# Performance work log

Measured on AMD Instinct MI355X. Metric: run time of the kernel, lower is better.

## Reference

```python
import jax, jax.numpy as jnp
import numpy as np

H = 4096
IN = 512
OUT = 64


def setup_inputs() -> dict:
    key = jax.random.key(0)
    ks = jax.random.split(key, 10)
    return {
        "inp": jax.random.normal(ks[0], (1, IN), jnp.float32),
        "hidden": jax.random.normal(ks[1], (1, H), jnp.float32),
        "hebb": jax.random.normal(ks[2], (H, H), jnp.float32) * 0.01,
        "W_i2h": jax.random.normal(ks[3], (H, IN), jnp.float32) * (1.0 / np.sqrt(IN)),
        "b_i2h": jax.random.normal(ks[4], (H,), jnp.float32),
        "w": jax.random.uniform(ks[5], (H, H), jnp.float32) * 0.01,
        "plas": jax.random.uniform(ks[6], (H, H), jnp.float32) * 0.01,
        "learn": jnp.full((1,), 0.01, jnp.float32),
        "W_h2o": jax.random.normal(ks[7], (OUT, H), jnp.float32) * (1.0 / np.sqrt(H)),
        "b_h2o": jax.random.normal(ks[8], (OUT,), jnp.float32),
    }


def reference(inp, hidden, hebb, W_i2h, b_i2h, w, plas, learn, W_h2o, b_h2o):
    # plastic-Miconi, rule='hebb', activ='relu'
    # x = relu(i2h(input) + hidden @ (w + plas * hebb))   [1, H]
    pre = inp @ W_i2h.T + b_i2h + hidden @ (w + plas * hebb)
    x = jax.nn.relu(pre)
    # hebb <- (1 - learn) * hebb + learn * outer(hidden, x)   [H, H]
    hebb_new = (1.0 - learn) * hebb + learn * (hidden.T @ x)
    # output = tanh(h2o(x))   [1, OUT]
    out = jnp.tanh(x @ W_h2o.T + b_h2o)
    return out, x, hebb_new
```

## Files before the change

kernel.cpp:

```cpp
#include <hip/hip_runtime.h>
#include <math.h>

#define H 4096
#define INP 512
#define OUTN 64
#define H4 (H / 4)
#define SPLITS 1024
#define RPS (H / SPLITS)

typedef float fx4 __attribute__((ext_vector_type(4)));

__global__ __launch_bounds__(256) void k_partial(
    const float* __restrict__ hidden,
    const float* __restrict__ w,
    const float* __restrict__ plas,
    const float* __restrict__ hebb,
    float* __restrict__ partial)
{
    const int t  = threadIdx.x;
    const int s  = blockIdx.x;
    const int i0 = s * RPS;
    const fx4* __restrict__ w4 = (const fx4*)w;
    const fx4* __restrict__ p4 = (const fx4*)plas;
    const fx4* __restrict__ h4 = (const fx4*)hebb;

    const float hv0 = hidden[i0 + 0];
    const float hv1 = hidden[i0 + 1];
    const float hv2 = hidden[i0 + 2];
    const float hv3 = hidden[i0 + 3];

    fx4 hbA[4], wvA[4], pvA[4];
    fx4 hbB[4], wvB[4], pvB[4];
    fx4 acc[4];
#pragma unroll
    for (int q = 0; q < 4; ++q) acc[q] = (fx4)(0.f);

    const size_t r0 = (size_t)i0 * H4 + t;

#define STAGE(dsth, dstw, dstp, row)                                   \
    _Pragma("unroll")                                                  \
    for (int q = 0; q < 4; ++q) {                                      \
        const size_t idx = r0 + (size_t)(row) * H4 + q * 256;          \
        dsth[q] = h4[idx];                                             \
        dstw[q] = __builtin_nontemporal_load(w4 + idx);                \
        dstp[q] = __builtin_nontemporal_load(p4 + idx);                \
    }

#define COMPUTE(hb, wv, pv, hv)                                        \
    _Pragma("unroll")                                                  \
    for (int q = 0; q < 4; ++q)                                        \
        acc[q] += (hv) * (wv[q] + pv[q] * hb[q]);

    STAGE(hbA, wvA, pvA, 0)
    STAGE(hbB, wvB, pvB, 1)
    __builtin_amdgcn_sched_barrier(0);
    COMPUTE(hbA, wvA, pvA, hv0)
    STAGE(hbA, wvA, pvA, 2)
    __builtin_amdgcn_sched_barrier(0);
    COMPUTE(hbB, wvB, pvB, hv1)
    STAGE(hbB, wvB, pvB, 3)
    __builtin_amdgcn_sched_barrier(0);
    COMPUTE(hbA, wvA, pvA, hv2)
    COMPUTE(hbB, wvB, pvB, hv3)
#undef STAGE
#undef COMPUTE

    fx4* __restrict__ o4 = (fx4*)partial + (size_t)s * H4 + t;
#pragma unroll
    for (int q = 0; q < 4; ++q)
        o4[q * 256] = acc[q];
}

__global__ __launch_bounds__(1024) void k_reduce_x(
    const float* __restrict__ partial,
    const float* __restrict__ inp,
    const float* __restrict__ W_i2h,
    const float* __restrict__ b_i2h,
    float* __restrict__ x_out)
{
    const int jl  = threadIdx.x & 31;
    const int grp = threadIdx.x >> 5;
    const int j   = blockIdx.x * 32 + jl;

    float sum = 0.f;
    const float* __restrict__ p = partial + (size_t)grp * (SPLITS / 32) * H + j;
#pragma unroll
    for (int s = 0; s < SPLITS / 32; ++s)
        sum += p[(size_t)s * H];

    const fx4* __restrict__ row4 = (const fx4*)(W_i2h + (size_t)j * INP);
    const fx4* __restrict__ in4  = (const fx4*)inp;
#pragma unroll
    for (int c = 0; c < 4; ++c) {
        const fx4 a = row4[grp * 4 + c];
        const fx4 b = in4[grp * 4 + c];
        sum += a.x * b.x + a.y * b.y + a.z * b.z + a.w * b.w;
    }

    __shared__ float red[32][33];
    red[grp][jl] = sum;
    __syncthreads();
    if (threadIdx.x < 32) {
        float tsum = 0.f;
#pragma unroll
        for (int g = 0; g < 32; ++g) tsum += red[g][jl];
        const float pre = tsum + b_i2h[j];
        x_out[j] = pre > 0.f ? pre : 0.f;
    }
}

__global__ __launch_bounds__(256) void k_tail(
    const float* __restrict__ hebb,
    const float* __restrict__ hidden,
    const float* __restrict__ x,
    const float* __restrict__ learn,
    const float* __restrict__ W_h2o,
    const float* __restrict__ b_h2o,
    float* __restrict__ hebb_out,
    float* __restrict__ out)
{
    if (blockIdx.x < H) {
        const int i = blockIdx.x;
        const float lr   = learn[0];
        const float om   = 1.f - lr;
        const float coef = lr * hidden[i];
        const fx4* __restrict__ hb4 = (const fx4*)hebb + (size_t)i * H4;
        const fx4* __restrict__ xx4 = (const fx4*)x;
        fx4* __restrict__ o4 = (fx4*)hebb_out + (size_t)i * H4;

        const int t = threadIdx.x;
        fx4 a[4], xv[4];
#pragma unroll
        for (int q = 0; q < 4; ++q) {
            a[q]  = hb4[t + q * 256];
            xv[q] = xx4[t + q * 256];
        }
        __builtin_amdgcn_sched_barrier(0);
#pragma unroll
        for (int q = 0; q < 4; ++q)
            __builtin_nontemporal_store(om * a[q] + coef * xv[q], o4 + t + q * 256);
    } else {
        const int o = blockIdx.x - H;
        const fx4* __restrict__ row4 = (const fx4*)(W_h2o + (size_t)o * H);
        const fx4* __restrict__ x4   = (const fx4*)x;
        float sum = 0.f;
#pragma unroll
        for (int c = threadIdx.x; c < H4; c += 256) {
            const fx4 a = row4[c];
            const fx4 b = x4[c];
            sum += a.x * b.x + a.y * b.y + a.z * b.z + a.w * b.w;
        }
#pragma unroll
        for (int off = 32; off > 0; off >>= 1)
            sum += __shfl_down(sum, off, 64);
        __shared__ float red[4];
        const int lane = threadIdx.x & 63;
        const int wave = threadIdx.x >> 6;
        if (lane == 0) red[wave] = sum;
        __syncthreads();
        if (threadIdx.x == 0) {
            const float ssum = red[0] + red[1] + red[2] + red[3];
            out[o] = tanhf(ssum + b_h2o[o]);
        }
    }
}

extern "C" void kernel_launch(void* const* d_in, const int* in_sizes, int n_in,
                              void* d_out, int out_size, void* d_ws, size_t ws_size,
                              hipStream_t stream)
{
    const float* inp    = (const float*)d_in[0];
    const float* hidden = (const float*)d_in[1];
    const float* hebb   = (const float*)d_in[2];
    const float* W_i2h  = (const float*)d_in[3];
    const float* b_i2h  = (const float*)d_in[4];
    const float* w      = (const float*)d_in[5];
    const float* plas   = (const float*)d_in[6];
    const float* learn  = (const float*)d_in[7];
    const float* W_h2o  = (const float*)d_in[8];
    const float* b_h2o  = (const float*)d_in[9];

    float* out      = (float*)d_out;
    float* x        = out + OUTN;
    float* hebb_out = x + H;

    const size_t part_bytes = (size_t)SPLITS * H * sizeof(float);
    float* partial = (ws_size >= part_bytes) ? (float*)d_ws : hebb_out;

    k_partial<<<SPLITS, 256, 0, stream>>>(hidden, w, plas, hebb, partial);
    k_reduce_x<<<H / 32, 1024, 0, stream>>>(partial, inp, W_i2h, b_i2h, x);
    k_tail<<<H + OUTN, 256, 0, stream>>>(hebb, hidden, x, learn, W_h2o, b_h2o, hebb_out, out);
}
```

Measured before the change: 246.4 us.

## Fuse all stages into one cooperative kernel with grid-wide syncs

Replaces the three-launch pipeline with a single cooperative kernel of 256 blocks x 1024 threads. The kernel computes per-block partial sums of hidden@(w+plas*hebb), runs a grid sync, reduces them to x, syncs again, and then computes the output and the hebb update. This removes two kernel launches and shrinks the partial buffer to 256 rows. The cost is grid-sync overhead and only 256 blocks to stream about 200MB of matrices, which may lower memory-level parallelism compared to the software-pipelined loads it replaces. The fallback kernels are also simplified and are used only if the cooperative launch fails.

```diff
diff --git a/kernel.cpp b/kernel.cpp
--- a/kernel.cpp
+++ b/kernel.cpp
@@ -1,14 +1,126 @@
 #include <hip/hip_runtime.h>
+#include <hip/hip_cooperative_groups.h>
 #include <math.h>
 
 #define H 4096
 #define INP 512
 #define OUTN 64
 #define H4 (H / 4)
+#define NB 256
+#define NT_ 1024
+#define RPB (H / NB)
+
+typedef float fx4 __attribute__((ext_vector_type(4)));
+
+namespace cg = cooperative_groups;
+
+__global__ __launch_bounds__(NT_) void k_fused(
+    const float* __restrict__ inp,
+    const float* __restrict__ hidden,
+    const float* __restrict__ hebb,
+    const float* __restrict__ W_i2h,
+    const float* __restrict__ b_i2h,
+    const float* __restrict__ w,
+    const float* __restrict__ plas,
+    const float* __restrict__ learn,
+    const float* __restrict__ W_h2o,
+    const float* __restrict__ b_h2o,
+    float* __restrict__ partial,
+    float* __restrict__ x,
+    float* __restrict__ hebb_out,
+    float* __restrict__ out)
+{
+    cg::grid_group grid = cg::this_grid();
+    const int t  = threadIdx.x;
+    const int b  = blockIdx.x;
+    const int i0 = b * RPB;
+
+    const fx4* __restrict__ w4 = (const fx4*)w;
+    const fx4* __restrict__ p4 = (const fx4*)plas;
+    const fx4* __restrict__ h4 = (const fx4*)hebb;
+
+    fx4 acc = (fx4)(0.f);
+    {
+        size_t idx = (size_t)i0 * H4 + t;
+#pragma unroll 4
+        for (int r = 0; r < RPB; ++r) {
+            const float hv = hidden[i0 + r];
+            const fx4 hb = h4[idx];
+            const fx4 wv = __builtin_nontemporal_load(w4 + idx);
+            const fx4 pv = __builtin_nontemporal_load(p4 + idx);
+            acc += hv * (wv + pv * hb);
+            idx += H4;
+        }
+    }
+    ((fx4*)partial)[(size_t)b * H4 + t] = acc;
+
+    grid.sync();
+
+    {
+        const int jj = t >> 6;
+        const int l  = t & 63;
+        const int j  = b * 16 + jj;
+        float sum = 0.f;
+#pragma unroll
+        for (int k = 0; k < 4; ++k)
+            sum += partial[(size_t)(l + 64 * k) * H + j];
+
+        const fx4* __restrict__ row4 = (const fx4*)(W_i2h + (size_t)j * INP);
+        const fx4* __restrict__ in4  = (const fx4*)inp;
+        const fx4 a0 = row4[l * 2],     a1 = row4[l * 2 + 1];
+        const fx4 c0 = in4[l * 2],      c1 = in4[l * 2 + 1];
+        sum += a0.x * c0.x + a0.y * c0.y + a0.z * c0.z + a0.w * c0.w
+             + a1.x * c1.x + a1.y * c1.y + a1.z * c1.z + a1.w * c1.w;
+
+#pragma unroll
+        for (int off = 32; off > 0; off >>= 1)
+            sum += __shfl_down(sum, off, 64);
+        if (l == 0) {
+            const float pre = sum + b_i2h[j];
+            x[j] = pre > 0.f ? pre : 0.f;
+        }
+    }
+
+    grid.sync();
+
+    const fx4* __restrict__ x4 = (const fx4*)x;
+
+    if (b < OUTN) {
+        const fx4* __restrict__ row4 = (const fx4*)(W_h2o + (size_t)b * H);
+        const fx4 aa = row4[t];
+        const fx4 xx = x4[t];
+        float s = aa.x * xx.x + aa.y * xx.y + aa.z * xx.z + aa.w * xx.w;
+#pragma unroll
+        for (int off = 32; off > 0; off >>= 1)
+            s += __shfl_down(s, off, 64);
+        __shared__ float red[NT_ / 64];
+        if ((t & 63) == 0) red[t >> 6] = s;
+        __syncthreads();
+        if (t == 0) {
+            float tot = 0.f;
+#pragma unroll
+            for (int u = 0; u < NT_ / 64; ++u) tot += red[u];
+            out[b] = tanhf(tot + b_h2o[b]);
+        }
+    }
+
+    {
+        const float lr   = learn[0];
+        const float om   = 1.f - lr;
+        const fx4 xt = x4[t];
+        size_t idx = (size_t)i0 * H4 + t;
+#pragma unroll 4
+        for (int r = 0; r < RPB; ++r) {
+            const float coef = lr * hidden[i0 + r];
+            const fx4 hb = h4[idx];
+            __builtin_nontemporal_store(om * hb + coef * xt, (fx4*)hebb_out + idx);
+            idx += H4;
+        }
+    }
+}
+
 #define SPLITS 1024
 #define RPS (H / SPLITS)
-
-typedef float fx4 __attribute__((ext_vector_type(4)));
 
 __global__ __launch_bounds__(256) void k_partial(
     const float* __restrict__ hidden,
@@ -24,51 +136,25 @@
     const fx4* __restrict__ p4 = (const fx4*)plas;
     const fx4* __restrict__ h4 = (const fx4*)hebb;
 
-    const float hv0 = hidden[i0 + 0];
-    const float hv1 = hidden[i0 + 1];
-    const float hv2 = hidden[i0 + 2];
-    const float hv3 = hidden[i0 + 3];
-
-    fx4 hbA[4], wvA[4], pvA[4];
-    fx4 hbB[4], wvB[4], pvB[4];
     fx4 acc[4];
 #pragma unroll
     for (int q = 0; q < 4; ++q) acc[q] = (fx4)(0.f);
-
     const size_t r0 = (size_t)i0 * H4 + t;
-
-#define STAGE(dsth, dstw, dstp, row)                                   \
-    _Pragma("unroll")                                                  \
-    for (int q = 0; q < 4; ++q) {                                      \
-        const size_t idx = r0 + (size_t)(row) * H4 + q * 256;          \
-        dsth[q] = h4[idx];                                             \
-        dstw[q] = __builtin_nontemporal_load(w4 + idx);                \
-        dstp[q] = __builtin_nontemporal_load(p4 + idx);                \
-    }
-
-#define COMPUTE(hb, wv, pv, hv)                                        \
-    _Pragma("unroll")                                                  \
-    for (int q = 0; q < 4; ++q)                                        \
-        acc[q] += (hv) * (wv[q] + pv[q] * hb[q]);
-
-    STAGE(hbA, wvA, pvA, 0)
-    STAGE(hbB, wvB, pvB, 1)
-    __builtin_amdgcn_sched_barrier(0);
-    COMPUTE(hbA, wvA, pvA, hv0)
-    STAGE(hbA, wvA, pvA, 2)
-    __builtin_amdgcn_sched_barrier(0);
-    COMPUTE(hbB, wvB, pvB, hv1)
-    STAGE(hbB, wvB, pvB, 3)
-    __builtin_amdgcn_sched_barrier(0);
-    COMPUTE(hbA, wvA, pvA, hv2)
-    COMPUTE(hbB, wvB, pvB, hv3)
-#undef STAGE
-#undef COMPUTE
-
+#pragma unroll
+    for (int r = 0; r < RPS; ++r) {
+        const float hv = hidden[i0 + r];
+#pragma unroll
+        for (int q = 0; q < 4; ++q) {
+            const size_t idx = r0 + (size_t)r * H4 + q * 256;
+            const fx4 hb = h4[idx];
+            const fx4 wv = __builtin_nontemporal_load(w4 + idx);
+            const fx4 pv = __builtin_nontemporal_load(p4 + idx);
+            acc[q] += hv * (wv + pv * hb);
+        }
+    }
     fx4* __restrict__ o4 = (fx4*)partial + (size_t)s * H4 + t;
 #pragma unroll
-    for (int q = 0; q < 4; ++q)
-        o4[q * 256] = acc[q];
+    for (int q = 0; q < 4; ++q) o4[q * 256] = acc[q];
 }
 
 __global__ __launch_bounds__(1024) void k_reduce_x(
@@ -81,13 +167,11 @@
     const int jl  = threadIdx.x & 31;
     const int grp = threadIdx.x >> 5;
     const int j   = blockIdx.x * 32 + jl;
-
     float sum = 0.f;
     const float* __restrict__ p = partial + (size_t)grp * (SPLITS / 32) * H + j;
 #pragma unroll
     for (int s = 0; s < SPLITS / 32; ++s)
         sum += p[(size_t)s * H];
-
     const fx4* __restrict__ row4 = (const fx4*)(W_i2h + (size_t)j * INP);
     const fx4* __restrict__ in4  = (const fx4*)inp;
 #pragma unroll
@@ -96,7 +180,6 @@
         const fx4 b = in4[grp * 4 + c];
         sum += a.x * b.x + a.y * b.y + a.z * b.z + a.w * b.w;
     }
-
     __shared__ float red[32][33];
     red[grp][jl] = sum;
     __syncthreads();
@@ -127,18 +210,11 @@
         const fx4* __restrict__ hb4 = (const fx4*)hebb + (size_t)i * H4;
         const fx4* __restrict__ xx4 = (const fx4*)x;
         fx4* __restrict__ o4 = (fx4*)hebb_out + (size_t)i * H4;
-
         const int t = threadIdx.x;
-        fx4 a[4], xv[4];
-#pragma unroll
-        for (int q = 0; q < 4; ++q) {
-            a[q]  = hb4[t + q * 256];
-            xv[q] = xx4[t + q * 256];
-        }
-        __builtin_amdgcn_sched_barrier(0);
 #pragma unroll
         for (int q = 0; q < 4; ++q)
-            __builtin_nontemporal_store(om * a[q] + coef * xv[q], o4 + t + q * 256);
+            __builtin_nontemporal_store(om * hb4[t + q * 256] + coef * xx4[t + q * 256],
+                                        o4 + t + q * 256);
     } else {
         const int o = blockIdx.x - H;
         const fx4* __restrict__ row4 = (const fx4*)(W_h2o + (size_t)o * H);
@@ -184,10 +260,22 @@
     float* x        = out + OUTN;
     float* hebb_out = x + H;
 
+    const size_t part_bytes_fused = (size_t)NB * H * sizeof(float);
+    float* partial = (ws_size >= part_bytes_fused) ? (float*)d_ws : hebb_out;
+
+    void* args[] = {
+        (void*)&inp, (void*)&hidden, (void*)&hebb, (void*)&W_i2h, (void*)&b_i2h,
+        (void*)&w, (void*)&plas, (void*)&learn, (void*)&W_h2o, (void*)&b_h2o,
+        (void*)&partial, (void*)&x, (void*)&hebb_out, (void*)&out
+    };
+    hipError_t err = hipLaunchCooperativeKernel((const void*)k_fused,
+                                                dim3(NB), dim3(NT_),
+                                                args, 0, stream);
+    if (err == hipSuccess) return;
+
     const size_t part_bytes = (size_t)SPLITS * H * sizeof(float);
-    float* partial = (ws_size >= part_bytes) ? (float*)d_ws : hebb_out;
-
-    k_partial<<<SPLITS, 256, 0, stream>>>(hidden, w, plas, hebb, partial);
-    k_reduce_x<<<H / 32, 1024, 0, stream>>>(partial, inp, W_i2h, b_i2h, x);
+    float* partial2 = (ws_size >= part_bytes) ? (float*)d_ws : hebb_out;
+    k_partial<<<SPLITS, 256, 0, stream>>>(hidden, w, plas, hebb, partial2);
+    k_reduce_x<<<H / 32, 1024, 0, stream>>>(partial2, inp, W_i2h, b_i2h, x);
     k_tail<<<H + OUTN, 256, 0, stream>>>(hebb, hidden, x, learn, W_h2o, b_h2o, hebb_out, out);
 }
```

Result: slower. 318.4 us (+29.2%).
